# Kernel tuning notes

Hardware: AMD Instinct MI355X
Metric: run time of the kernel (lower is better)

The kernel has to match this reference:

```python
import jax, jax.numpy as jnp
import numpy as np

T, B, H, L = 1024, 64, 512, 2
IN = 512  # input_size == hidden_size so layer weights stack
GATE = 3 * H  # fixed-forget subLSTM: in_gate, out_gate, z


def setup_inputs() -> dict:
    key = jax.random.key(0)
    ks = jax.random.split(key, 6)
    stdv = 1.0 / np.sqrt(H)
    u = lambda k, shape: jax.random.uniform(k, shape, jnp.float32, -stdv, stdv)
    return {
        "x": jax.random.normal(ks[0], (T, B, IN), jnp.float32),
        "h0": jnp.zeros((L, B, H), jnp.float32),
        "c0": jnp.zeros((L, B, H), jnp.float32),
        "W": u(ks[1], (L, GATE, IN)),
        "R": u(ks[2], (L, GATE, H)),
        "bi": u(ks[3], (L, GATE)),
        "bh": u(ks[4], (L, GATE)),
        "f": u(ks[5], (L, H)),
    }


def reference(x, h0, c0, W, R, bi, bh, f):
    num_layers = W.shape[0]
    fg = jax.nn.sigmoid(f)  # fixed forget gate per layer/unit, [L, H]

    def step(carry, x_t):
        h, c = carry  # each [L, B, H]
        inp = x_t  # [B, IN]
        new_h, new_c = [], []
        for l in range(num_layers):
            proj = jax.nn.sigmoid(inp @ W[l].T + bi[l] + h[l] @ R[l].T + bh[l])
            i_g, o_g, z = jnp.split(proj, 3, axis=-1)
            c_t = c[l] * fg[l] + z - i_g
            h_t = jax.nn.sigmoid(c_t) - o_g
            new_h.append(h_t)
            new_c.append(c_t)
            inp = h_t
        return (jnp.stack(new_h), jnp.stack(new_c)), inp

    (h_f, c_f), output = jax.lax.scan(step, (h0, c0), x)
    return output, h_f, c_f
```

## Files before the change

### kernel.cpp

```cpp
#include <hip/hip_runtime.h>
#include <hip/hip_bf16.h>
#include <stdint.h>


#define TSTEPS 1024
#define BATCH  64
#define HID    512
#define GATE   1536
#define GROWS  8
#define NT     256
#define NBLOCKS 256

typedef unsigned long long u64;
typedef __attribute__((ext_vector_type(8))) short short8;
typedef __attribute__((ext_vector_type(4))) short short4v;
typedef __attribute__((ext_vector_type(4))) float floatx4;

__device__ __forceinline__ float sigmoidf_(float x) { return 1.0f / (1.0f + __expf(-x)); }

__device__ __forceinline__ unsigned short f2bf(float x) {
    union { float f; unsigned u; } v; v.f = x;
    unsigned r = v.u + 0x7FFFu + ((v.u >> 16) & 1u);
    return (unsigned short)(r >> 16);
}

__device__ __forceinline__ short8 load_frag(const float* p) {
    floatx4 a = *(const floatx4*)p;
    floatx4 b = *(const floatx4*)(p + 4);
    short8 r;
#pragma unroll
    for (int j = 0; j < 4; ++j) { r[j] = (short)f2bf(a[j]); r[j+4] = (short)f2bf(b[j]); }
    return r;
}

__device__ __forceinline__ u64 ring_ld(const u64* p) {
    return __hip_atomic_load(p, __ATOMIC_RELAXED, __HIP_MEMORY_SCOPE_AGENT);
}
__device__ __forceinline__ void ring_st(u64* p, u64 v) {
    __hip_atomic_store(p, v, __ATOMIC_RELAXED, __HIP_MEMORY_SCOPE_AGENT);
}

__global__ __launch_bounds__(256) void xconvert(const float* __restrict__ x,
                                                unsigned short* __restrict__ xb) {
    const size_t i = ((size_t)blockIdx.x*256 + threadIdx.x) * 8;
    floatx4 a = *(const floatx4*)(x + i);
    floatx4 b = *(const floatx4*)(x + i + 4);
    short8 p;
#pragma unroll
    for (int j = 0; j < 4; ++j) { p[j] = (short)f2bf(a[j]); p[j+4] = (short)f2bf(b[j]); }
    *(short8*)(xb + i) = p;
}

__global__ __launch_bounds__(NT, 1) void sublstm_fused(
    const unsigned short* __restrict__ xb,
    const float* __restrict__ W,
    const float* __restrict__ R,
    const float* __restrict__ bi,
    const float* __restrict__ bh,
    const float* __restrict__ fw,
    const float* __restrict__ h0,
    const float* __restrict__ c0,
    u64* __restrict__ ring,
    float* __restrict__ out)
{
    const int tid  = threadIdx.x;
    const int lane = tid & 63;
    const int wid  = tid >> 6;
    const int bid  = blockIdx.x;
    const int g    = bid & 7;
    const int bidx = bid >> 3;
    const int col0 = bidx << 4;

    __shared__ __align__(16) unsigned short x_tile[16][520];
    __shared__ __align__(16) unsigned short hA[16][520];
    __shared__ __align__(16) unsigned short hB[16][520];
    __shared__ float proj[3][16][17];

    for (int i = tid; i < 16*520; i += NT) {
        ((unsigned short*)x_tile)[i] = 0;
        ((unsigned short*)hA)[i] = 0;
        ((unsigned short*)hB)[i] = 0;
    }
    __syncthreads();

    const int lrow = lane & 15;
    const int lk   = (lane >> 4) << 3;

    short8 wf0[16], rf0[16], wf1[16], rf1[16];
    float bias0 = 0.f, bias1 = 0.f;
    if (wid < 3) {
        const int wrow = wid*HID + col0 + lrow;
#pragma unroll
        for (int kc = 0; kc < 16; ++kc) {
            wf0[kc] = load_frag(W + (size_t)wrow*HID + kc*32 + lk);
            rf0[kc] = load_frag(R + (size_t)wrow*HID + kc*32 + lk);
            wf1[kc] = load_frag(W + ((size_t)GATE + wrow)*HID + kc*32 + lk);
            rf1[kc] = load_frag(R + ((size_t)GATE + wrow)*HID + kc*32 + lk);
        }
        bias0 = bi[wrow] + bh[wrow];
        bias1 = bi[GATE + wrow] + bh[GATE + wrow];
    }

    const int lyr  = tid >> 7;
    const int srow = (tid >> 4) & 7;
    const int scol = tid & 15;
    const float fgv = sigmoidf_(fw[(size_t)lyr*HID + col0 + scol]);
    float creg = c0[((size_t)lyr*BATCH + g*GROWS + srow)*HID + col0 + scol];

    {
        const unsigned short* xp = xb + (size_t)g*GROWS*HID;
        for (int w = tid; w < GROWS*HID/8; w += NT) {
            const int r = w >> 6, c8 = (w & 63) << 3;
            *(short8*)(&x_tile[r][c8]) = *(const short8*)(xp + (size_t)r*HID + c8);
        }
        const float* hp0 = h0 + (size_t)g*GROWS*HID;
        const float* hp1 = h0 + ((size_t)BATCH + g*GROWS)*HID;
        for (int w = tid; w < GROWS*HID/4; w += NT) {
            const int r = w >> 7, c4 = (w & 127) << 2;
            floatx4 va_ = *(const floatx4*)(hp0 + (size_t)r*HID + c4);
            floatx4 vb_ = *(const floatx4*)(hp1 + (size_t)r*HID + c4);
            short4v pa, pb;
#pragma unroll
            for (int j = 0; j < 4; ++j) { pa[j] = (short)f2bf(va_[j]); pb[j] = (short)f2bf(vb_[j]); }
            *(short4v*)(&hA[r][c4]) = pa;
            *(short4v*)(&hB[r][c4]) = pb;
        }
    }
    __syncthreads();

    floatx4 a0a_sav = {0,0,0,0};
    if (wid < 3) {
#pragma unroll
        for (int kc = 0; kc < 16; ++kc) {
            short8 afx = *(const short8*)(&x_tile[lrow][kc*32 + lk]);
            a0a_sav = __builtin_amdgcn_mfma_f32_16x16x32_bf16(afx, wf0[kc], a0a_sav, 0, 0, 0);
        }
    }
    short8 xr0, xr1;
    {
        const unsigned short* xp = xb + (size_t)BATCH*HID + (size_t)g*GROWS*HID;
        xr0 = *(const short8*)(xp + (size_t)(tid >> 6)*HID + ((tid & 63) << 3));
        const int w1 = tid + 256;
        xr1 = *(const short8*)(xp + (size_t)(w1 >> 6)*HID + ((w1 & 63) << 3));
    }

    int budget = 1 << 22;
    int pend_t = -1;
    float pend_h = 0.f, pend_c = 0.f;
    u64 va0[8], va1[8];

    for (int i = 0; i <= TSTEPS; ++i) {
        if (i >= 1) {
            const unsigned want = (unsigned)i;
            const u64* rb0 = ring + ((size_t)((i - 1) & 3)*8 + g)*2048;
            unsigned stale = 0;
#pragma unroll
            for (int k = 0; k < 8; ++k)
                if ((unsigned)(va0[k] >> 32) != want) stale |= (1u << k);
            int pass = 0;
            while (__any((int)(stale != 0)) && budget > 0) {
                if (pass++) __builtin_amdgcn_s_sleep(1);
#pragma unroll
                for (int k = 0; k < 8; ++k)
                    if (stale & (1u << k)) va0[k] = ring_ld(rb0 + tid + (k << 8));
#pragma unroll
                for (int k = 0; k < 8; ++k)
                    if (stale & (1u << k))
                        if ((unsigned)(va0[k] >> 32) == want) stale &= ~(1u << k);
                --budget;
            }
#pragma unroll
            for (int k = 0; k < 8; ++k) {
                const int w = tid + (k << 8);
                const int b = w >> 6, r = (w >> 3) & 7, u = w & 7;
                *(unsigned*)(&hA[r][b*16 + u*2]) = (unsigned)va0[k];
            }
        }
        __syncthreads();

        if (wid < 3 && i < TSTEPS) {
            floatx4 ae = {0,0,0,0}, ao = {0,0,0,0};
#pragma unroll
            for (int kc = 0; kc < 16; kc += 2) {
                short8 h0f = *(const short8*)(&hA[lrow][kc*32 + lk]);
                short8 h1f = *(const short8*)(&hA[lrow][(kc+1)*32 + lk]);
                ae = __builtin_amdgcn_mfma_f32_16x16x32_bf16(h0f, rf0[kc],   ae, 0, 0, 0);
                ao = __builtin_amdgcn_mfma_f32_16x16x32_bf16(h1f, rf0[kc+1], ao, 0, 0, 0);
            }
            const int erow0 = (lane >> 4) << 2, ecol = lrow;
#pragma unroll
            for (int q = 0; q < 4; ++q)
                proj[wid][erow0 + q][ecol] = sigmoidf_(a0a_sav[q] + ae[q] + ao[q] + bias0);
        }
        __syncthreads();

        if (i >= 2) {
            const u64* rb1 = ring + ((size_t)(4 + ((i - 2) & 3))*8 + g)*2048;
#pragma unroll
            for (int k = 0; k < 8; ++k)
                va1[k] = ring_ld(rb1 + tid + (k << 8));
        }
        __builtin_amdgcn_sched_barrier(0);

        if (lyr == 0 && i < TSTEPS) {
            const float ig = proj[0][srow][scol];
            const float og = proj[1][srow][scol];
            const float zz = proj[2][srow][scol];
            const float c_ = creg*fgv + zz - ig;
            creg = c_;
            const float h_ = sigmoidf_(c_) - og;
            const unsigned hu = __float_as_uint(h_);
            const unsigned pu = (unsigned)__builtin_amdgcn_ds_swizzle((int)hu, 0x041F);
            unsigned pay;
            asm volatile("v_cvt_pk_bf16_f32 %0, %1, %2"
                         : "=v"(pay) : "v"(h_), "v"(__uint_as_float(pu)));
            if (!(scol & 1)) {
                const size_t off = (((size_t)(i & 3)*8 + g)*32 + bidx)*64
                                 + srow*8 + (scol >> 1);
                ring_st(ring + off, (u64)pay | ((u64)(unsigned)(i + 1) << 32));
            }
            if (i == TSTEPS - 1) { pend_t = i; pend_h = h_; pend_c = c_; }
        }
        __builtin_amdgcn_sched_barrier(0);

        floatx4 a1a = {0,0,0,0};
        if (wid < 3 && i >= 1) {
#pragma unroll
            for (int kc = 0; kc < 16; ++kc) {
                short8 afh = *(const short8*)(&hA[lrow][kc*32 + lk]);
                a1a = __builtin_amdgcn_mfma_f32_16x16x32_bf16(afh, wf1[kc], a1a, 0, 0, 0);
            }
        }
        __builtin_amdgcn_sched_barrier(0);

        if (i >= 2) {
            const unsigned want = (unsigned)(i - 1);
            const u64* rb1 = ring + ((size_t)(4 + ((i - 2) & 3))*8 + g)*2048;
            unsigned stale = 0;
#pragma unroll
            for (int k = 0; k < 8; ++k)
                if ((unsigned)(va1[k] >> 32) != want) stale |= (1u << k);
            int pass = 0;
            while (__any((int)(stale != 0)) && budget > 0) {
                if (pass++) __builtin_amdgcn_s_sleep(1);
#pragma unroll
                for (int k = 0; k < 8; ++k)
                    if (stale & (1u << k)) va1[k] = ring_ld(rb1 + tid + (k << 8));
#pragma unroll
                for (int k = 0; k < 8; ++k)
                    if (stale & (1u << k))
                        if ((unsigned)(va1[k] >> 32) == want) stale &= ~(1u << k);
                --budget;
            }
#pragma unroll
            for (int k = 0; k < 8; ++k) {
                const int w = tid + (k << 8);
                const int b = w >> 6, r = (w >> 3) & 7, u = w & 7;
                *(unsigned*)(&hB[r][b*16 + u*2]) = (unsigned)va1[k];
            }
        }
        if (i + 1 < TSTEPS) {
            *(short8*)(&x_tile[tid >> 6][(tid & 63) << 3]) = xr0;
            const int w1 = tid + 256;
            *(short8*)(&x_tile[w1 >> 6][(w1 & 63) << 3]) = xr1;
        }
        if (i + 2 < TSTEPS) {
            const unsigned short* xp = xb + ((size_t)(i + 2)*BATCH + g*GROWS)*HID;
            xr0 = *(const short8*)(xp + (size_t)(tid >> 6)*HID + ((tid & 63) << 3));
            const int w1 = tid + 256;
            xr1 = *(const short8*)(xp + (size_t)(w1 >> 6)*HID + ((w1 & 63) << 3));
        }
        if (pend_t >= 0) {
            if (lyr == 1)
                out[((size_t)pend_t*BATCH + g*GROWS + srow)*HID + col0 + scol] = pend_h;
            if (pend_t == TSTEPS - 1) {
                const size_t fo = (size_t)TSTEPS*BATCH*HID
                                + ((size_t)lyr*BATCH + g*GROWS + srow)*HID + col0 + scol;
                out[fo] = pend_h;
                out[fo + (size_t)2*BATCH*HID] = pend_c;
            }
            pend_t = -1;
        }
        __syncthreads();

        if (wid < 3 && i >= 1) {
            floatx4 be = {0,0,0,0}, bo = {0,0,0,0};
#pragma unroll
            for (int kc = 0; kc < 16; kc += 2) {
                short8 b0f = *(const short8*)(&hB[lrow][kc*32 + lk]);
                short8 b1f = *(const short8*)(&hB[lrow][(kc+1)*32 + lk]);
                be = __builtin_amdgcn_mfma_f32_16x16x32_bf16(b0f, rf1[kc],   be, 0, 0, 0);
                bo = __builtin_amdgcn_mfma_f32_16x16x32_bf16(b1f, rf1[kc+1], bo, 0, 0, 0);
            }
            const int erow0 = (lane >> 4) << 2, ecol = lrow;
#pragma unroll
            for (int q = 0; q < 4; ++q)
                proj[wid][erow0 + q][ecol] = sigmoidf_(a1a[q] + be[q] + bo[q] + bias1);
        }
        if (i < TSTEPS) {
            const u64* rb0n = ring + ((size_t)(i & 3)*8 + g)*2048;
#pragma unroll
            for (int k = 0; k < 8; ++k)
                va0[k] = ring_ld(rb0n + tid + (k << 8));
        }
        __syncthreads();

        if (lyr == 1 && i >= 1) {
            const int t = i - 1;
            const float ig = proj[0][srow][scol];
            const float og = proj[1][srow][scol];
            const float zz = proj[2][srow][scol];
            const float c_ = creg*fgv + zz - ig;
            creg = c_;
            const float h_ = sigmoidf_(c_) - og;
            const unsigned hu = __float_as_uint(h_);
            const unsigned pu = (unsigned)__builtin_amdgcn_ds_swizzle((int)hu, 0x041F);
            unsigned pay;
            asm volatile("v_cvt_pk_bf16_f32 %0, %1, %2"
                         : "=v"(pay) : "v"(h_), "v"(__uint_as_float(pu)));
            if (!(scol & 1)) {
                const size_t off = (((size_t)(4 + (t & 3))*8 + g)*32 + bidx)*64
                                 + srow*8 + (scol >> 1);
                ring_st(ring + off, (u64)pay | ((u64)(unsigned)(t + 1) << 32));
            }
            pend_t = t; pend_h = h_; pend_c = c_;
        }

        if (wid < 3 && i + 1 < TSTEPS) {
            floatx4 an = {0,0,0,0};
#pragma unroll
            for (int kc = 0; kc < 16; ++kc) {
                short8 afx = *(const short8*)(&x_tile[lrow][kc*32 + lk]);
                an = __builtin_amdgcn_mfma_f32_16x16x32_bf16(afx, wf0[kc], an, 0, 0, 0);
            }
            a0a_sav = an;
        }
    }

    if (pend_t >= 0) {
        if (lyr == 1)
            out[((size_t)pend_t*BATCH + g*GROWS + srow)*HID + col0 + scol] = pend_h;
        if (pend_t == TSTEPS - 1) {
            const size_t fo = (size_t)TSTEPS*BATCH*HID
                            + ((size_t)lyr*BATCH + g*GROWS + srow)*HID + col0 + scol;
            out[fo] = pend_h;
            out[fo + (size_t)2*BATCH*HID] = pend_c;
        }
    }
}

extern "C" void kernel_launch(void* const* d_in, const int* in_sizes, int n_in,
                              void* d_out, int out_size, void* d_ws, size_t ws_size,
                              hipStream_t stream)
{
    (void)in_sizes; (void)n_in; (void)out_size; (void)ws_size;
    const float* x  = (const float*)d_in[0];
    const float* h0 = (const float*)d_in[1];
    const float* c0 = (const float*)d_in[2];
    const float* W  = (const float*)d_in[3];
    const float* R  = (const float*)d_in[4];
    const float* bi = (const float*)d_in[5];
    const float* bh = (const float*)d_in[6];
    const float* fw = (const float*)d_in[7];
    float* out = (float*)d_out;

    u64* ring = (u64*)d_ws;
    unsigned short* xbuf = (unsigned short*)((char*)d_ws + (2u << 20));

    hipMemsetAsync(d_ws, 0, (size_t)2*4*8*2048*8, stream);

    xconvert<<<dim3(TSTEPS*BATCH*HID/(256*8)), dim3(256), 0, stream>>>(x, xbuf);

    sublstm_fused<<<dim3(NBLOCKS), dim3(NT), 0, stream>>>(
        xbuf, W, R, bi, bh, fw, h0, c0, ring, out);
}
```

Before: 3.429 ms.

## Split layers across separate persistent blocks with flag-based layer pipelining

Before, each persistent block computed both layers in lockstep. Now 512 blocks run, half for layer 0 and half for layer 1, each holding only its own layer's weights in registers. Layer 0 can run up to 8 steps ahead through a deeper ring buffer, gated by progress counters that layer 1 publishes. This is meant to overlap the two layers' recurrences and shorten each block's per-step critical path. The cost is twice as many co-resident blocks, which must all fit at once (launch bounds now allow 2 per CU), plus extra cross-block polling traffic.

Measured after the change: 5.999 ms. 1.75x slower.

```diff
diff --git a/kernel.cpp b/kernel.cpp
--- a/kernel.cpp
+++ b/kernel.cpp
@@ -9,7 +9,6 @@
 #define GATE   1536
 #define GROWS  8
 #define NT     256
-#define NBLOCKS 256
 
 typedef unsigned long long u64;
 typedef __attribute__((ext_vector_type(8))) short short8;
@@ -37,6 +36,12 @@
     return __hip_atomic_load(p, __ATOMIC_RELAXED, __HIP_MEMORY_SCOPE_AGENT);
 }
 __device__ __forceinline__ void ring_st(u64* p, u64 v) {
+    __hip_atomic_store(p, v, __ATOMIC_RELAXED, __HIP_MEMORY_SCOPE_AGENT);
+}
+__device__ __forceinline__ unsigned prog_ld(const unsigned* p) {
+    return __hip_atomic_load(p, __ATOMIC_RELAXED, __HIP_MEMORY_SCOPE_AGENT);
+}
+__device__ __forceinline__ void prog_st(unsigned* p, unsigned v) {
     __hip_atomic_store(p, v, __ATOMIC_RELAXED, __HIP_MEMORY_SCOPE_AGENT);
 }
 
@@ -51,7 +56,7 @@
     *(short8*)(xb + i) = p;
 }
 
-__global__ __launch_bounds__(NT, 1) void sublstm_fused(
+__global__ __launch_bounds__(NT, 2) void sublstm_split(
     const unsigned short* __restrict__ xb,
     const float* __restrict__ W,
     const float* __restrict__ R,
@@ -60,289 +65,317 @@
     const float* __restrict__ fw,
     const float* __restrict__ h0,
     const float* __restrict__ c0,
-    u64* __restrict__ ring,
+    u64* __restrict__ ring0,
+    u64* __restrict__ ring1,
+    unsigned* __restrict__ prog,
     float* __restrict__ out)
 {
     const int tid  = threadIdx.x;
     const int lane = tid & 63;
     const int wid  = tid >> 6;
     const int bid  = blockIdx.x;
-    const int g    = bid & 7;
-    const int bidx = bid >> 3;
+    const bool isL0 = (bid < 256);
+    const int b    = isL0 ? bid : (bid - 256);
+    const int g    = b & 7;
+    const int bidx = b >> 3;
     const int col0 = bidx << 4;
 
-    __shared__ __align__(16) unsigned short x_tile[16][520];
-    __shared__ __align__(16) unsigned short hA[16][520];
-    __shared__ __align__(16) unsigned short hB[16][520];
+    __shared__ __align__(16) unsigned short tA[16][520];
+    __shared__ __align__(16) unsigned short tB[16][520];
     __shared__ float proj[3][16][17];
 
     for (int i = tid; i < 16*520; i += NT) {
-        ((unsigned short*)x_tile)[i] = 0;
-        ((unsigned short*)hA)[i] = 0;
-        ((unsigned short*)hB)[i] = 0;
+        ((unsigned short*)tA)[i] = 0;
+        ((unsigned short*)tB)[i] = 0;
     }
     __syncthreads();
 
     const int lrow = lane & 15;
     const int lk   = (lane >> 4) << 3;
 
-    short8 wf0[16], rf0[16], wf1[16], rf1[16];
-    float bias0 = 0.f, bias1 = 0.f;
+    short8 wa[16], wb[16];
+    float bias = 0.f;
     if (wid < 3) {
+        const size_t lo = isL0 ? 0 : (size_t)GATE;
         const int wrow = wid*HID + col0 + lrow;
 #pragma unroll
         for (int kc = 0; kc < 16; ++kc) {
-            wf0[kc] = load_frag(W + (size_t)wrow*HID + kc*32 + lk);
-            rf0[kc] = load_frag(R + (size_t)wrow*HID + kc*32 + lk);
-            wf1[kc] = load_frag(W + ((size_t)GATE + wrow)*HID + kc*32 + lk);
-            rf1[kc] = load_frag(R + ((size_t)GATE + wrow)*HID + kc*32 + lk);
-        }
-        bias0 = bi[wrow] + bh[wrow];
-        bias1 = bi[GATE + wrow] + bh[GATE + wrow];
-    }
-
-    const int lyr  = tid >> 7;
+            wa[kc] = load_frag(W + (lo + wrow)*HID + kc*32 + lk);
+            wb[kc] = load_frag(R + (lo + wrow)*HID + kc*32 + lk);
+        }
+        bias = bi[lo + wrow] + bh[lo + wrow];
+    }
+
+    const bool active = (tid < 128);
     const int srow = (tid >> 4) & 7;
     const int scol = tid & 15;
+    const int lyr  = isL0 ? 0 : 1;
     const float fgv = sigmoidf_(fw[(size_t)lyr*HID + col0 + scol]);
-    float creg = c0[((size_t)lyr*BATCH + g*GROWS + srow)*HID + col0 + scol];
-
-    {
+    float creg = active ? c0[((size_t)lyr*BATCH + g*GROWS + srow)*HID + col0 + scol] : 0.f;
+
+    if (isL0) {
         const unsigned short* xp = xb + (size_t)g*GROWS*HID;
         for (int w = tid; w < GROWS*HID/8; w += NT) {
             const int r = w >> 6, c8 = (w & 63) << 3;
-            *(short8*)(&x_tile[r][c8]) = *(const short8*)(xp + (size_t)r*HID + c8);
-        }
-        const float* hp0 = h0 + (size_t)g*GROWS*HID;
-        const float* hp1 = h0 + ((size_t)BATCH + g*GROWS)*HID;
+            *(short8*)(&tA[r][c8]) = *(const short8*)(xp + (size_t)r*HID + c8);
+        }
+        const float* hp = h0 + (size_t)g*GROWS*HID;
         for (int w = tid; w < GROWS*HID/4; w += NT) {
             const int r = w >> 7, c4 = (w & 127) << 2;
-            floatx4 va_ = *(const floatx4*)(hp0 + (size_t)r*HID + c4);
-            floatx4 vb_ = *(const floatx4*)(hp1 + (size_t)r*HID + c4);
-            short4v pa, pb;
-#pragma unroll
-            for (int j = 0; j < 4; ++j) { pa[j] = (short)f2bf(va_[j]); pb[j] = (short)f2bf(vb_[j]); }
-            *(short4v*)(&hA[r][c4]) = pa;
-            *(short4v*)(&hB[r][c4]) = pb;
+            floatx4 v = *(const floatx4*)(hp + (size_t)r*HID + c4);
+            short4v p4;
+#pragma unroll
+            for (int j = 0; j < 4; ++j) p4[j] = (short)f2bf(v[j]);
+            *(short4v*)(&tB[r][c4]) = p4;
+        }
+    } else {
+        const float* hp = h0 + ((size_t)BATCH + g*GROWS)*HID;
+        for (int w = tid; w < GROWS*HID/4; w += NT) {
+            const int r = w >> 7, c4 = (w & 127) << 2;
+            floatx4 v = *(const floatx4*)(hp + (size_t)r*HID + c4);
+            short4v p4;
+#pragma unroll
+            for (int j = 0; j < 4; ++j) p4[j] = (short)f2bf(v[j]);
+            *(short4v*)(&tB[r][c4]) = p4;
         }
     }
     __syncthreads();
 
     floatx4 a0a_sav = {0,0,0,0};
-    if (wid < 3) {
-#pragma unroll
-        for (int kc = 0; kc < 16; ++kc) {
-            short8 afx = *(const short8*)(&x_tile[lrow][kc*32 + lk]);
-            a0a_sav = __builtin_amdgcn_mfma_f32_16x16x32_bf16(afx, wf0[kc], a0a_sav, 0, 0, 0);
-        }
-    }
     short8 xr0, xr1;
-    {
+    u64 va[16];
+    if (isL0) {
+        if (wid < 3) {
+#pragma unroll
+            for (int kc = 0; kc < 16; ++kc) {
+                short8 afx = *(const short8*)(&tA[lrow][kc*32 + lk]);
+                a0a_sav = __builtin_amdgcn_mfma_f32_16x16x32_bf16(afx, wa[kc], a0a_sav, 0, 0, 0);
+            }
+        }
         const unsigned short* xp = xb + (size_t)BATCH*HID + (size_t)g*GROWS*HID;
         xr0 = *(const short8*)(xp + (size_t)(tid >> 6)*HID + ((tid & 63) << 3));
         const int w1 = tid + 256;
         xr1 = *(const short8*)(xp + (size_t)(w1 >> 6)*HID + ((w1 & 63) << 3));
+    } else {
+        const u64* rb = ring0 + (size_t)g*2048;
+#pragma unroll
+        for (int k = 0; k < 8; ++k) va[k] = ring_ld(rb + tid + (k << 8));
     }
 
     int budget = 1 << 22;
     int pend_t = -1;
     float pend_h = 0.f, pend_c = 0.f;
-    u64 va0[8], va1[8];
-
-    for (int i = 0; i <= TSTEPS; ++i) {
-        if (i >= 1) {
-            const unsigned want = (unsigned)i;
-            const u64* rb0 = ring + ((size_t)((i - 1) & 3)*8 + g)*2048;
-            unsigned stale = 0;
-#pragma unroll
-            for (int k = 0; k < 8; ++k)
-                if ((unsigned)(va0[k] >> 32) != want) stale |= (1u << k);
-            int pass = 0;
-            while (__any((int)(stale != 0)) && budget > 0) {
-                if (pass++) __builtin_amdgcn_s_sleep(1);
+
+    for (int t = 0; t < TSTEPS; ++t) {
+        if (isL0) {
+            if (t >= 1) {
+                const unsigned want = (unsigned)t;
+                const u64* rb = ring0 + ((size_t)((t - 1) & 7)*8 + g)*2048;
+                unsigned stale = 0;
 #pragma unroll
                 for (int k = 0; k < 8; ++k)
-                    if (stale & (1u << k)) va0[k] = ring_ld(rb0 + tid + (k << 8));
-#pragma unroll
-                for (int k = 0; k < 8; ++k)
-                    if (stale & (1u << k))
-                        if ((unsigned)(va0[k] >> 32) == want) stale &= ~(1u << k);
-                --budget;
-            }
-#pragma unroll
-            for (int k = 0; k < 8; ++k) {
-                const int w = tid + (k << 8);
-                const int b = w >> 6, r = (w >> 3) & 7, u = w & 7;
-                *(unsigned*)(&hA[r][b*16 + u*2]) = (unsigned)va0[k];
-            }
-        }
-        __syncthreads();
-
-        if (wid < 3 && i < TSTEPS) {
+                    if ((unsigned)(va[k] >> 32) != want) stale |= (1u << k);
+                int pass = 0;
+                while (__any((int)(stale != 0)) && budget > 0) {
+                    if (pass++) __builtin_amdgcn_s_sleep(1);
+#pragma unroll
+                    for (int k = 0; k < 8; ++k)
+                        if (stale & (1u << k)) va[k] = ring_ld(rb + tid + (k << 8));
+#pragma unroll
+                    for (int k = 0; k < 8; ++k)
+                        if (stale & (1u << k))
+                            if ((unsigned)(va[k] >> 32) == want) stale &= ~(1u << k);
+                    --budget;
+                }
+#pragma unroll
+                for (int k = 0; k < 8; ++k) {
+                    const int w = tid + (k << 8);
+                    const int bb = w >> 6, r = (w >> 3) & 7, u = w & 7;
+                    *(unsigned*)(&tB[r][bb*16 + u*2]) = (unsigned)va[k];
+                }
+            }
+            __syncthreads();
+
+            if (t + 1 < TSTEPS) {
+                *(short8*)(&tA[tid >> 6][(tid & 63) << 3]) = xr0;
+                const int w1 = tid + 256;
+                *(short8*)(&tA[w1 >> 6][(w1 & 63) << 3]) = xr1;
+            }
+            if (wid == 3 && t >= 8) {
+                const unsigned* pp = prog + (size_t)g*32*4;
+                while (budget > 0) {
+                    unsigned v = 0xFFFFFFFFu;
+                    if (lane < 32) v = prog_ld(pp + (size_t)lane*4);
+                    if (__all((int)((lane >= 32) || ((int)v >= t - 7)))) break;
+                    __builtin_amdgcn_s_sleep(1);
+                    --budget;
+                }
+            }
             floatx4 ae = {0,0,0,0}, ao = {0,0,0,0};
-#pragma unroll
-            for (int kc = 0; kc < 16; kc += 2) {
-                short8 h0f = *(const short8*)(&hA[lrow][kc*32 + lk]);
-                short8 h1f = *(const short8*)(&hA[lrow][(kc+1)*32 + lk]);
-                ae = __builtin_amdgcn_mfma_f32_16x16x32_bf16(h0f, rf0[kc],   ae, 0, 0, 0);
-                ao = __builtin_amdgcn_mfma_f32_16x16x32_bf16(h1f, rf0[kc+1], ao, 0, 0, 0);
-            }
-            const int erow0 = (lane >> 4) << 2, ecol = lrow;
-#pragma unroll
-            for (int q = 0; q < 4; ++q)
-                proj[wid][erow0 + q][ecol] = sigmoidf_(a0a_sav[q] + ae[q] + ao[q] + bias0);
-        }
-        __syncthreads();
-
-        if (i >= 2) {
-            const u64* rb1 = ring + ((size_t)(4 + ((i - 2) & 3))*8 + g)*2048;
-#pragma unroll
-            for (int k = 0; k < 8; ++k)
-                va1[k] = ring_ld(rb1 + tid + (k << 8));
-        }
-        __builtin_amdgcn_sched_barrier(0);
-
-        if (lyr == 0 && i < TSTEPS) {
-            const float ig = proj[0][srow][scol];
-            const float og = proj[1][srow][scol];
-            const float zz = proj[2][srow][scol];
-            const float c_ = creg*fgv + zz - ig;
-            creg = c_;
-            const float h_ = sigmoidf_(c_) - og;
-            const unsigned hu = __float_as_uint(h_);
-            const unsigned pu = (unsigned)__builtin_amdgcn_ds_swizzle((int)hu, 0x041F);
-            unsigned pay;
-            asm volatile("v_cvt_pk_bf16_f32 %0, %1, %2"
-                         : "=v"(pay) : "v"(h_), "v"(__uint_as_float(pu)));
-            if (!(scol & 1)) {
-                const size_t off = (((size_t)(i & 3)*8 + g)*32 + bidx)*64
-                                 + srow*8 + (scol >> 1);
-                ring_st(ring + off, (u64)pay | ((u64)(unsigned)(i + 1) << 32));
-            }
-            if (i == TSTEPS - 1) { pend_t = i; pend_h = h_; pend_c = c_; }
-        }
-        __builtin_amdgcn_sched_barrier(0);
-
-        floatx4 a1a = {0,0,0,0};
-        if (wid < 3 && i >= 1) {
-#pragma unroll
-            for (int kc = 0; kc < 16; ++kc) {
-                short8 afh = *(const short8*)(&hA[lrow][kc*32 + lk]);
-                a1a = __builtin_amdgcn_mfma_f32_16x16x32_bf16(afh, wf1[kc], a1a, 0, 0, 0);
-            }
-        }
-        __builtin_amdgcn_sched_barrier(0);
-
-        if (i >= 2) {
-            const unsigned want = (unsigned)(i - 1);
-            const u64* rb1 = ring + ((size_t)(4 + ((i - 2) & 3))*8 + g)*2048;
-            unsigned stale = 0;
-#pragma unroll
-            for (int k = 0; k < 8; ++k)
-                if ((unsigned)(va1[k] >> 32) != want) stale |= (1u << k);
-            int pass = 0;
-            while (__any((int)(stale != 0)) && budget > 0) {
-                if (pass++) __builtin_amdgcn_s_sleep(1);
-#pragma unroll
-                for (int k = 0; k < 8; ++k)
-                    if (stale & (1u << k)) va1[k] = ring_ld(rb1 + tid + (k << 8));
-#pragma unroll
-                for (int k = 0; k < 8; ++k)
-                    if (stale & (1u << k))
-                        if ((unsigned)(va1[k] >> 32) == want) stale &= ~(1u << k);
-                --budget;
-            }
-#pragma unroll
-            for (int k = 0; k < 8; ++k) {
-                const int w = tid + (k << 8);
-                const int b = w >> 6, r = (w >> 3) & 7, u = w & 7;
-                *(unsigned*)(&hB[r][b*16 + u*2]) = (unsigned)va1[k];
-            }
-        }
-        if (i + 1 < TSTEPS) {
-            *(short8*)(&x_tile[tid >> 6][(tid & 63) << 3]) = xr0;
-            const int w1 = tid + 256;
-            *(short8*)(&x_tile[w1 >> 6][(w1 & 63) << 3]) = xr1;
-        }
-        if (i + 2 < TSTEPS) {
-            const unsigned short* xp = xb + ((size_t)(i + 2)*BATCH + g*GROWS)*HID;
-            xr0 = *(const short8*)(xp + (size_t)(tid >> 6)*HID + ((tid & 63) << 3));
-            const int w1 = tid + 256;
-            xr1 = *(const short8*)(xp + (size_t)(w1 >> 6)*HID + ((w1 & 63) << 3));
-        }
-        if (pend_t >= 0) {
-            if (lyr == 1)
+            if (wid < 3) {
+#pragma unroll
+                for (int kc = 0; kc < 16; kc += 2) {
+                    short8 h0f = *(const short8*)(&tB[lrow][kc*32 + lk]);
+                    short8 h1f = *(const short8*)(&tB[lrow][(kc+1)*32 + lk]);
+                    ae = __builtin_amdgcn_mfma_f32_16x16x32_bf16(h0f, wb[kc],   ae, 0, 0, 0);
+                    ao = __builtin_amdgcn_mfma_f32_16x16x32_bf16(h1f, wb[kc+1], ao, 0, 0, 0);
+                }
+                const int erow0 = (lane >> 4) << 2, ecol = lrow;
+#pragma unroll
+                for (int q = 0; q < 4; ++q)
+                    proj[wid][erow0 + q][ecol] = sigmoidf_(a0a_sav[q] + ae[q] + ao[q] + bias);
+            }
+            __syncthreads();
+
+            if (active) {
+                const float ig = proj[0][srow][scol];
+                const float og = proj[1][srow][scol];
+                const float zz = proj[2][srow][scol];
+                const float c_ = creg*fgv + zz - ig;
+                creg = c_;
+                const float h_ = sigmoidf_(c_) - og;
+                const unsigned hu = __float_as_uint(h_);
+                const unsigned pu = (unsigned)__builtin_amdgcn_ds_swizzle((int)hu, 0x041F);
+                unsigned pay;
+                asm volatile("v_cvt_pk_bf16_f32 %0, %1, %2"
+                             : "=v"(pay) : "v"(h_), "v"(__uint_as_float(pu)));
+                if (!(scol & 1)) {
+                    const size_t off = (((size_t)(t & 7)*8 + g)*32 + bidx)*64
+                                     + srow*8 + (scol >> 1);
+                    ring_st(ring0 + off, (u64)pay | ((u64)(unsigned)(t + 1) << 32));
+                }
+                if (t == TSTEPS - 1) {
+                    const size_t fo = (size_t)TSTEPS*BATCH*HID
+                                    + ((size_t)g*GROWS + srow)*HID + col0 + scol;
+                    out[fo] = h_;
+                    out[fo + (size_t)2*BATCH*HID] = c_;
+                }
+            }
+            if (wid < 3 && t + 1 < TSTEPS) {
+                floatx4 an = {0,0,0,0};
+#pragma unroll
+                for (int kc = 0; kc < 16; ++kc) {
+                    short8 afx = *(const short8*)(&tA[lrow][kc*32 + lk]);
+                    an = __builtin_amdgcn_mfma_f32_16x16x32_bf16(afx, wa[kc], an, 0, 0, 0);
+                }
+                a0a_sav = an;
+            }
+            if (t + 2 < TSTEPS) {
+                const unsigned short* xp = xb + ((size_t)(t + 2)*BATCH + g*GROWS)*HID;
+                xr0 = *(const short8*)(xp + (size_t)(tid >> 6)*HID + ((tid & 63) << 3));
+                const int w1 = tid + 256;
+                xr1 = *(const short8*)(xp + (size_t)(w1 >> 6)*HID + ((w1 & 63) << 3));
+            }
+            if (t + 1 < TSTEPS) {
+                const u64* rb = ring0 + ((size_t)(t & 7)*8 + g)*2048;
+#pragma unroll
+                for (int k = 0; k < 8; ++k) va[k] = ring_ld(rb + tid + (k << 8));
+            }
+        } else {
+            if (pend_t >= 0) {
                 out[((size_t)pend_t*BATCH + g*GROWS + srow)*HID + col0 + scol] = pend_h;
-            if (pend_t == TSTEPS - 1) {
-                const size_t fo = (size_t)TSTEPS*BATCH*HID
-                                + ((size_t)lyr*BATCH + g*GROWS + srow)*HID + col0 + scol;
-                out[fo] = pend_h;
-                out[fo + (size_t)2*BATCH*HID] = pend_c;
-            }
-            pend_t = -1;
-        }
-        __syncthreads();
-
-        if (wid < 3 && i >= 1) {
-            floatx4 be = {0,0,0,0}, bo = {0,0,0,0};
-#pragma unroll
-            for (int kc = 0; kc < 16; kc += 2) {
-                short8 b0f = *(const short8*)(&hB[lrow][kc*32 + lk]);
-                short8 b1f = *(const short8*)(&hB[lrow][(kc+1)*32 + lk]);
-                be = __builtin_amdgcn_mfma_f32_16x16x32_bf16(b0f, rf1[kc],   be, 0, 0, 0);
-                bo = __builtin_amdgcn_mfma_f32_16x16x32_bf16(b1f, rf1[kc+1], bo, 0, 0, 0);
-            }
-            const int erow0 = (lane >> 4) << 2, ecol = lrow;
-#pragma unroll
-            for (int q = 0; q < 4; ++q)
-                proj[wid][erow0 + q][ecol] = sigmoidf_(a1a[q] + be[q] + bo[q] + bias1);
-        }
-        if (i < TSTEPS) {
-            const u64* rb0n = ring + ((size_t)(i & 3)*8 + g)*2048;
-#pragma unroll
-            for (int k = 0; k < 8; ++k)
-                va0[k] = ring_ld(rb0n + tid + (k << 8));
-        }
-        __syncthreads();
-
-        if (lyr == 1 && i >= 1) {
-            const int t = i - 1;
-            const float ig = proj[0][srow][scol];
-            const float og = proj[1][srow][scol];
-            const float zz = proj[2][srow][scol];
-            const float c_ = creg*fgv + zz - ig;
-            creg = c_;
-            const float h_ = sigmoidf_(c_) - og;
-            const unsigned hu = __float_as_uint(h_);
-            const unsigned pu = (unsigned)__builtin_amdgcn_ds_swizzle((int)hu, 0x041F);
-            unsigned pay;
-            asm volatile("v_cvt_pk_bf16_f32 %0, %1, %2"
-                         : "=v"(pay) : "v"(h_), "v"(__uint_as_float(pu)));
-            if (!(scol & 1)) {
-                const size_t off = (((size_t)(4 + (t & 3))*8 + g)*32 + bidx)*64
-                                 + srow*8 + (scol >> 1);
-                ring_st(ring + off, (u64)pay | ((u64)(unsigned)(t + 1) << 32));
-            }
-            pend_t = t; pend_h = h_; pend_c = c_;
-        }
-
-        if (wid < 3 && i + 1 < TSTEPS) {
-            floatx4 an = {0,0,0,0};
-#pragma unroll
-            for (int kc = 0; kc < 16; ++kc) {
-                short8 afx = *(const short8*)(&x_tile[lrow][kc*32 + lk]);
-                an = __builtin_amdgcn_mfma_f32_16x16x32_bf16(afx, wf0[kc], an, 0, 0, 0);
-            }
-            a0a_sav = an;
-        }
-    }
-
-    if (pend_t >= 0) {
-        if (lyr == 1)
-            out[((size_t)pend_t*BATCH + g*GROWS + srow)*HID + col0 + scol] = pend_h;
+                pend_t = -1;
+            }
+            {
+                const unsigned wantF = (unsigned)(t + 1);
+                const unsigned wantB = (unsigned)t;
+                const int kmax = (t >= 1) ? 16 : 8;
+                const u64* rbF = ring0 + ((size_t)(t & 7)*8 + g)*2048;
+                const u64* rbB = ring1 + ((size_t)((t - 1) & 3)*8 + g)*2048;
+                unsigned stale = 0;
+#pragma unroll
+                for (int k = 0; k < 16; ++k)
+                    if (k < kmax)
+                        if ((unsigned)(va[k] >> 32) != ((k < 8) ? wantF : wantB))
+                            stale |= (1u << k);
+                int pass = 0;
+                while (__any((int)(stale != 0)) && budget > 0) {
+                    if (pass++) __builtin_amdgcn_s_sleep(1);
+#pragma unroll
+                    for (int k = 0; k < 16; ++k)
+                        if (k < kmax && (stale & (1u << k)))
+                            va[k] = ring_ld((k < 8) ? (rbF + tid + (k << 8))
+                                                    : (rbB + tid + ((k - 8) << 8)));
+#pragma unroll
+                    for (int k = 0; k < 16; ++k)
+                        if (k < kmax && (stale & (1u << k)))
+                            if ((unsigned)(va[k] >> 32) == ((k < 8) ? wantF : wantB))
+                                stale &= ~(1u << k);
+                    --budget;
+                }
+#pragma unroll
+                for (int k = 0; k < 16; ++k) {
+                    if (k < kmax) {
+                        const int w = tid + ((k & 7) << 8);
+                        const int bb = w >> 6, r = (w >> 3) & 7, u = w & 7;
+                        unsigned* dst = (k < 8)
+                            ? (unsigned*)(&tA[r][bb*16 + u*2])
+                            : (unsigned*)(&tB[r][bb*16 + u*2]);
+                        *dst = (unsigned)va[k];
+                    }
+                }
+                if (tid == 0)
+                    prog_st(prog + ((size_t)g*32 + bidx)*4, (unsigned)(t + 1));
+            }
+            __syncthreads();
+
+            floatx4 fe = {0,0,0,0}, fo_ = {0,0,0,0}, be = {0,0,0,0}, bo = {0,0,0,0};
+            if (wid < 3) {
+#pragma unroll
+                for (int kc = 0; kc < 16; kc += 2) {
+                    short8 f0 = *(const short8*)(&tA[lrow][kc*32 + lk]);
+                    short8 f1 = *(const short8*)(&tA[lrow][(kc+1)*32 + lk]);
+                    short8 b0 = *(const short8*)(&tB[lrow][kc*32 + lk]);
+                    short8 b1 = *(const short8*)(&tB[lrow][(kc+1)*32 + lk]);
+                    fe  = __builtin_amdgcn_mfma_f32_16x16x32_bf16(f0, wa[kc],   fe,  0, 0, 0);
+                    fo_ = __builtin_amdgcn_mfma_f32_16x16x32_bf16(f1, wa[kc+1], fo_, 0, 0, 0);
+                    be  = __builtin_amdgcn_mfma_f32_16x16x32_bf16(b0, wb[kc],   be,  0, 0, 0);
+                    bo  = __builtin_amdgcn_mfma_f32_16x16x32_bf16(b1, wb[kc+1], bo,  0, 0, 0);
+                }
+                const int erow0 = (lane >> 4) << 2, ecol = lrow;
+#pragma unroll
+                for (int q = 0; q < 4; ++q)
+                    proj[wid][erow0 + q][ecol] =
+                        sigmoidf_(fe[q] + fo_[q] + be[q] + bo[q] + bias);
+            }
+            __syncthreads();
+
+            if (active) {
+                const float ig = proj[0][srow][scol];
+                const float og = proj[1][srow][scol];
+                const float zz = proj[2][srow][scol];
+                const float c_ = creg*fgv + zz - ig;
+                creg = c_;
+                const float h_ = sigmoidf_(c_) - og;
+                const unsigned hu = __float_as_uint(h_);
+                const unsigned pu = (unsigned)__builtin_amdgcn_ds_swizzle((int)hu, 0x041F);
+                unsigned pay;
+                asm volatile("v_cvt_pk_bf16_f32 %0, %1, %2"
+                             : "=v"(pay) : "v"(h_), "v"(__uint_as_float(pu)));
+                if (!(scol & 1)) {
+                    const size_t off = (((size_t)(t & 3)*8 + g)*32 + bidx)*64
+                                     + srow*8 + (scol >> 1);
+                    ring_st(ring1 + off, (u64)pay | ((u64)(unsigned)(t + 1) << 32));
+                }
+                pend_t = t; pend_h = h_; pend_c = c_;
+            }
+            if (t + 1 < TSTEPS) {
+                const u64* rbF = ring0 + ((size_t)((t + 1) & 7)*8 + g)*2048;
+                const u64* rbB = ring1 + ((size_t)(t & 3)*8 + g)*2048;
+#pragma unroll
+                for (int k = 0; k < 8; ++k) {
+                    va[k]     = ring_ld(rbF + tid + (k << 8));
+                    va[8 + k] = ring_ld(rbB + tid + (k << 8));
+                }
+            }
+        }
+    }
+
+    if (!isL0 && pend_t >= 0) {
+        out[((size_t)pend_t*BATCH + g*GROWS + srow)*HID + col0 + scol] = pend_h;
         if (pend_t == TSTEPS - 1) {
             const size_t fo = (size_t)TSTEPS*BATCH*HID
-                            + ((size_t)lyr*BATCH + g*GROWS + srow)*HID + col0 + scol;
+                            + ((size_t)BATCH + g*GROWS + srow)*HID + col0 + scol;
             out[fo] = pend_h;
             out[fo + (size_t)2*BATCH*HID] = pend_c;
         }
@@ -364,13 +397,15 @@
     const float* fw = (const float*)d_in[7];
     float* out = (float*)d_out;
 
-    u64* ring = (u64*)d_ws;
+    u64* ring0 = (u64*)d_ws;
+    u64* ring1 = (u64*)((char*)d_ws + (1u << 20));
+    unsigned* prog = (unsigned*)((char*)d_ws + 0x180000);
     unsigned short* xbuf = (unsigned short*)((char*)d_ws + (2u << 20));
 
-    hipMemsetAsync(d_ws, 0, (size_t)2*4*8*2048*8, stream);
+    hipMemsetAsync(d_ws, 0, 2u << 20, stream);
 
     xconvert<<<dim3(TSTEPS*BATCH*HID/(256*8)), dim3(256), 0, stream>>>(x, xbuf);
 
-    sublstm_fused<<<dim3(NBLOCKS), dim3(NT), 0, stream>>>(
-        xbuf, W, R, bi, bh, fw, h0, c0, ring, out);
-}
+    sublstm_split<<<dim3(512), dim3(NT), 0, stream>>>(
+        xbuf, W, R, bi, bh, fw, h0, c0, ring0, ring1, prog, out);
+}
```
